# Performance work log

Hardware: AMD Instinct MI355X
Metric: run time of the kernel (lower is better)

Reference implementation:

```python
import jax, jax.numpy as jnp
import numpy as np

EPS_LN = 1e-05   # LayerNorm eps in SimpleCogVideoXLayerNormZero
EPS_QK = 1e-06   # RMSNorm eps for qk_norm

DIM = 2048
FFN = 8192
HEADS = 16
HEAD_DIM = DIM // HEADS
TEMB = 512
F, H, W = 4, 24, 24
SEQ = F * H * W  # 2304
B = 1


def _layernorm(x, weight, bias, eps):
    mu = jnp.mean(x, axis=-1, keepdims=True)
    var = jnp.mean((x - mu) ** 2, axis=-1, keepdims=True)
    return (x - mu) * jax.lax.rsqrt(var + eps) * weight + bias


def _rmsnorm(x, weight, eps):
    var = jnp.mean(x * x, axis=-1, keepdims=True)
    return x * jax.lax.rsqrt(var + eps) * weight


def _ln_zero(x, temb, lin_w, lin_b, n_w, n_b):
    # shift/scale/gate modulation from temb
    t = jax.nn.silu(temb) @ lin_w + lin_b          # [B, 3*dim]
    shift, scale, gate = jnp.split(t, 3, axis=1)
    xn = _layernorm(x, n_w, n_b, EPS_LN)
    return xn * (1.0 + scale)[:, None, :] + shift[:, None, :], gate[:, None, :]


def _rope(x, cos, sin):
    # x: [B, S, H, D]; cos/sin: [S, 1, D] broadcastable
    x1 = x[..., 0::2]
    x2 = x[..., 1::2]
    c = cos[..., 0::2]
    s = sin[..., 1::2]
    even = x1 * c - x2 * s
    odd = x1 * s + x2 * c
    return jnp.stack([even, odd], axis=-1).reshape(x.shape)


def _forward(hidden_states, ref_states, temb, cos_h, sin_h, cos_r, sin_r,
             ln1_lw, ln1_lb, ln1_nw, ln1_nb, ln2_lw, ln2_lb, ln2_nw, ln2_nb,
             wq, bq, wk, bk, wv, bv, nq_w, nk_w, wo, bo,
             ffn_w1, ffn_b1, ffn_w2, ffn_b2, f, h, w):
    b, s, dim = hidden_states.shape
    heads = HEADS
    hd = dim // heads
    scale = hd ** -0.5

    def qkv(x, cos, sin):
        q = _rmsnorm(x @ wq + bq, nq_w, EPS_QK)
        k = _rmsnorm(x @ wk + bk, nk_w, EPS_QK)
        v = x @ wv + bv
        q = q.reshape(b, s, heads, hd)
        k = k.reshape(b, s, heads, hd)
        v = v.reshape(b, s, heads, hd)
        q = _rope(q, cos, sin)
        k = _rope(k, cos, sin)
        return q, k, v

    def attn(nh, nr):
        q, k, v = qkv(nh, cos_h, sin_h)
        rq, rk, rv = qkv(nr, cos_r, sin_r)

        def combine(a, ra):
            a = a.reshape(b, f, h, w, heads, hd)
            ra = ra.reshape(b, f, h, w, heads, hd)
            c = jnp.concatenate([a, ra], axis=3)          # [b,f,h,2w,H,D]
            return c.reshape(b * f, h * 2 * w, heads, hd)  # [(bf),(h 2w),H,D]

        cq, ck, cv = combine(q, rq), combine(k, rk), combine(v, rv)
        logits = jnp.einsum('bqhd,bkhd->bhqk', cq, ck) * scale
        probs = jax.nn.softmax(logits, axis=-1)
        out = jnp.einsum('bhqk,bkhd->bqhd', probs, cv)
        out = out.reshape(b, f, h, 2 * w, heads, hd)
        ah = out[:, :, :, :w].reshape(b, s, dim)
        ar = out[:, :, :, w:].reshape(b, s, dim)
        return ah @ wo + bo, ar @ wo + bo

    def ffn(x):
        return jax.nn.gelu(x @ ffn_w1 + ffn_b1, approximate=True) @ ffn_w2 + ffn_b2

    norm_h, gate_h = _ln_zero(hidden_states, temb, ln1_lw, ln1_lb, ln1_nw, ln1_nb)
    norm_r, gate_r = _ln_zero(ref_states, temb, ln1_lw, ln1_lb, ln1_nw, ln1_nb)
    attn_h, attn_r = attn(norm_h, norm_r)

    hidden_states = hidden_states + gate_h * attn_h
    norm_h2, gate_ff = _ln_zero(hidden_states, temb, ln2_lw, ln2_lb, ln2_nw, ln2_nb)
    ref_states = ref_states + gate_r * attn_r
    norm_r2, gate_ff_r = _ln_zero(ref_states, temb, ln2_lw, ln2_lb, ln2_nw, ln2_nb)

    hidden_states = hidden_states + gate_ff * ffn(norm_h2)
    ref_states = ref_states + gate_ff_r * ffn(norm_r2)
    return hidden_states, ref_states


def setup_inputs() -> dict:
    key = jax.random.key(0)
    ks = jax.random.split(key, 24)
    std = 0.02
    inp = {
        'hidden_states': jax.random.normal(ks[0], (B, SEQ, DIM), jnp.float32),
        'ref_states': jax.random.normal(ks[1], (B, SEQ, DIM), jnp.float32),
        'temb': jax.random.normal(ks[2], (B, TEMB), jnp.float32),
        'cos_h': jax.random.uniform(ks[3], (SEQ, 1, HEAD_DIM), jnp.float32),
        'sin_h': jax.random.uniform(ks[4], (SEQ, 1, HEAD_DIM), jnp.float32),
        'cos_r': jax.random.uniform(ks[5], (SEQ, 1, HEAD_DIM), jnp.float32),
        'sin_r': jax.random.uniform(ks[6], (SEQ, 1, HEAD_DIM), jnp.float32),
        'ln1_lw': jax.random.normal(ks[7], (TEMB, 3 * DIM), jnp.float32) * std,
        'ln1_lb': jnp.zeros((3 * DIM,), jnp.float32),
        'ln1_nw': jnp.ones((DIM,), jnp.float32),
        'ln1_nb': jnp.zeros((DIM,), jnp.float32),
        'ln2_lw': jax.random.normal(ks[8], (TEMB, 3 * DIM), jnp.float32) * std,
        'ln2_lb': jnp.zeros((3 * DIM,), jnp.float32),
        'ln2_nw': jnp.ones((DIM,), jnp.float32),
        'ln2_nb': jnp.zeros((DIM,), jnp.float32),
        'wq': jax.random.normal(ks[9], (DIM, DIM), jnp.float32) * std,
        'bq': jnp.zeros((DIM,), jnp.float32),
        'wk': jax.random.normal(ks[10], (DIM, DIM), jnp.float32) * std,
        'bk': jnp.zeros((DIM,), jnp.float32),
        'wv': jax.random.normal(ks[11], (DIM, DIM), jnp.float32) * std,
        'bv': jnp.zeros((DIM,), jnp.float32),
        'nq_w': jnp.ones((DIM,), jnp.float32),
        'nk_w': jnp.ones((DIM,), jnp.float32),
        'wo': jax.random.normal(ks[12], (DIM, DIM), jnp.float32) * std,
        'bo': jnp.zeros((DIM,), jnp.float32),
        'ffn_w1': jax.random.normal(ks[13], (DIM, FFN), jnp.float32) * std,
        'ffn_b1': jnp.zeros((FFN,), jnp.float32),
        'ffn_w2': jax.random.normal(ks[14], (FFN, DIM), jnp.float32) * std,
        'ffn_b2': jnp.zeros((DIM,), jnp.float32),
        'f': F, 'h': H, 'w': W,
    }
    return inp


def reference(hidden_states, ref_states, temb, cos_h, sin_h, cos_r, sin_r,
              ln1_lw, ln1_lb, ln1_nw, ln1_nb, ln2_lw, ln2_lb, ln2_nw, ln2_nb,
              wq, bq, wk, bk, wv, bv, nq_w, nk_w, wo, bo,
              ffn_w1, ffn_b1, ffn_w2, ffn_b2, f, h, w):
    return _forward(hidden_states, ref_states, temb, cos_h, sin_h, cos_r, sin_r,
                    ln1_lw, ln1_lb, ln1_nw, ln1_nb, ln2_lw, ln2_lb, ln2_nw, ln2_nb,
                    wq, bq, wk, bk, wv, bv, nq_w, nk_w, wo, bo,
                    ffn_w1, ffn_b1, ffn_w2, ffn_b2, f, h, w)
```

## Files before the change

kernel.cpp:

```cpp
#include <hip/hip_runtime.h>

typedef unsigned int u32;
typedef unsigned short us16;
typedef __bf16 bf16x8 __attribute__((ext_vector_type(8)));
typedef float f32x4 __attribute__((ext_vector_type(4)));

constexpr int S    = 2304;
constexpr int S2   = 4608;
constexpr int D    = 2048;
constexpr int NQKV = 3 * D;
constexpr int NH   = 16;
constexpr int HD   = 128;
constexpr int FFN  = 8192;
constexpr int CT   = 1152;
constexpr float ATTN_SCALE = 0.08838834764831845f;

__device__ __forceinline__ us16 f2bf(float f) {
  u32 x = __float_as_uint(f);
  x += 0x7fffu + ((x >> 16) & 1u);
  return (us16)(x >> 16);
}
__device__ __forceinline__ float blk_sum256(float v, float* red, int tid) {
  #pragma unroll
  for (int o = 32; o; o >>= 1) v += __shfl_down(v, o, 64);
  __syncthreads();
  if ((tid & 63) == 0) red[tid >> 6] = v;
  __syncthreads();
  return red[0] + red[1] + red[2] + red[3];
}

typedef const __attribute__((address_space(1))) void* gas_ptr;
typedef __attribute__((address_space(3))) void* las_ptr;
__device__ __forceinline__ void gload16(const us16* g, us16* l) {
  __builtin_amdgcn_global_load_lds((gas_ptr)g, (las_ptr)l, 16, 0, 0);
}

__device__ __forceinline__ float gelu_tanh(float x) {
  float y = 0.7978845608028654f * (x + 0.044715f * x * x * x);
  float e = __expf(2.0f * y);
  float t = 1.0f - 2.0f / (e + 1.0f);
  return 0.5f * x * (1.0f + t);
}

__global__ __launch_bounds__(256) void transpose_cvt(
    const float* __restrict__ in, us16* __restrict__ out, int Kd, int Nd) {
  __shared__ float tile[32][33];
  int tx = threadIdx.x, ty = threadIdx.y;
  int n0 = blockIdx.x * 32, k0 = blockIdx.y * 32;
  #pragma unroll
  for (int i = 0; i < 4; i++)
    tile[ty + i * 8][tx] = in[(size_t)(k0 + ty + i * 8) * Nd + n0 + tx];
  __syncthreads();
  #pragma unroll
  for (int i = 0; i < 4; i++)
    out[(size_t)(n0 + ty + i * 8) * Kd + k0 + tx] = f2bf(tile[tx][ty + i * 8]);
}

__global__ __launch_bounds__(256) void temb_mod(
    const float* __restrict__ temb,
    const float* __restrict__ lw1, const float* __restrict__ lb1,
    const float* __restrict__ lw2, const float* __restrict__ lb2,
    float* __restrict__ t1, float* __restrict__ t2) {
  __shared__ float st[512];
  int tid = threadIdx.x;
  for (int i = tid; i < 512; i += 256) {
    float v = temb[i];
    st[i] = v / (1.0f + __expf(-v));
  }
  __syncthreads();
  int which = blockIdx.x / 24;
  int n = (blockIdx.x % 24) * 256 + tid;
  const float* lw = which ? lw2 : lw1;
  const float* lb = which ? lb2 : lb1;
  float acc = lb[n];
  #pragma unroll 4
  for (int k = 0; k < 512; k++) acc += st[k] * lw[(size_t)k * (3 * D) + n];
  (which ? t2 : t1)[n] = acc;
}

__global__ __launch_bounds__(256) void ln_mod(
    const float* __restrict__ x, const float* __restrict__ t,
    const float* __restrict__ nw, const float* __restrict__ nb,
    us16* __restrict__ out) {
  __shared__ float red[4];
  int tok = blockIdx.x, tid = threadIdx.x;
  const float* xr = x + (size_t)tok * D;
  float v[8];
  float4 a = *(const float4*)(xr + tid * 8);
  float4 b = *(const float4*)(xr + tid * 8 + 4);
  v[0]=a.x; v[1]=a.y; v[2]=a.z; v[3]=a.w; v[4]=b.x; v[5]=b.y; v[6]=b.z; v[7]=b.w;
  float s = 0;
  #pragma unroll
  for (int i = 0; i < 8; i++) s += v[i];
  float mu = blk_sum256(s, red, tid) * (1.0f / D);
  float sq = 0;
  #pragma unroll
  for (int i = 0; i < 8; i++) { float d = v[i] - mu; sq += d * d; }
  float var = blk_sum256(sq, red, tid) * (1.0f / D);
  float rinv = rsqrtf(var + 1e-5f);
  int n = tid * 8;
  us16 o[8];
  #pragma unroll
  for (int i = 0; i < 8; i++) {
    float xn = (v[i] - mu) * rinv * nw[n + i] + nb[n + i];
    float y = xn * (1.0f + t[D + n + i]) + t[n + i];
    o[i] = f2bf(y);
  }
  *(uint4*)(out + (size_t)tok * D + n) = *(uint4*)o;
}

template <int EPI>
__global__ __launch_bounds__(256) void gemm128(
    const us16* __restrict__ A, const us16* __restrict__ BT,
    const float* __restrict__ b0, const float* __restrict__ b1,
    const float* __restrict__ b2, int bmask, void* __restrict__ Cout,
    int M, int N, int K) {
  __shared__ __align__(16) us16 As[128 * 32];
  __shared__ __align__(16) us16 Bs[128 * 32];
  const int tid = threadIdx.x;

  const int nbx = N >> 7;
  const int nwg = nbx * (M >> 7);
  int bid = (int)blockIdx.x;
  bid = (bid & 7) * (nwg >> 3) + (bid >> 3);
  const int by = bid / nbx;
  const int m0 = by << 7;
  const int n0 = (bid - by * nbx) << 7;

  const int srow = tid >> 2;
  const int scol = (tid & 3) << 3;
  const us16* Ap = A + (size_t)(m0 + srow) * K + scol;
  const us16* Bp = BT + (size_t)(n0 + srow) * K + scol;
  const size_t rstep = (size_t)64 * K;
  us16* lA = As + ((tid >> 6) << 9);
  us16* lB = Bs + ((tid >> 6) << 9);

  const int w = tid >> 6, l = tid & 63;
  const int wr = (w >> 1) << 6, wc = (w & 1) << 6;
  const int m = l & 15, quad = l >> 4;
  const us16* Ard = As + (wr + m) * 32 + quad * 8;
  const us16* Brd = Bs + (wc + m) * 32 + quad * 8;

  f32x4 acc[4][4] = {};
  for (int k0 = 0; k0 < K; k0 += 32) {
    __syncthreads();
    gload16(Ap + k0, lA);
    gload16(Ap + rstep + k0, lA + 2048);
    gload16(Bp + k0, lB);
    gload16(Bp + rstep + k0, lB + 2048);
    __syncthreads();
    bf16x8 af[4], bf[4];
    #pragma unroll
    for (int i = 0; i < 4; i++) {
      af[i] = *(const bf16x8*)(Ard + i * 512);
      bf[i] = *(const bf16x8*)(Brd + i * 512);
    }
    #pragma unroll
    for (int mi = 0; mi < 4; mi++)
      #pragma unroll
      for (int ni = 0; ni < 4; ni++)
        acc[mi][ni] = __builtin_amdgcn_mfma_f32_16x16x32_bf16(
            af[mi], bf[ni], acc[mi][ni], 0, 0, 0);
  }

  const float* bp = b0;
  if (b1) { int seg = (n0 + wc) >> 11; if (seg == 1) bp = b1; else if (seg >= 2) bp = b2; }

  const int r0 = m0 + wr + (quad << 2);
  #pragma unroll
  for (int ni = 0; ni < 4; ni++) {
    const int col = n0 + wc + ni * 16 + m;
    const float bv = bp ? bp[col & bmask] : 0.0f;
    #pragma unroll
    for (int mi = 0; mi < 4; mi++) {
      const int row = r0 + mi * 16;
      #pragma unroll
      for (int r = 0; r < 4; r++) {
        float y = acc[mi][ni][r] + bv;
        if constexpr (EPI == 1) {
          ((us16*)Cout)[(size_t)(row + r) * N + col] = f2bf(gelu_tanh(y));
        } else {
          ((float*)Cout)[(size_t)(row + r) * N + col] = y;
        }
      }
    }
  }
}

__global__ __launch_bounds__(256) void qkv_scatter(
    const float* __restrict__ raw, const float* __restrict__ nw,
    const float* __restrict__ cos_h, const float* __restrict__ sin_h,
    const float* __restrict__ cos_r, const float* __restrict__ sin_r,
    us16* __restrict__ out, int mode) {
  __shared__ float red[4];
  int t = blockIdx.x, tid = threadIdx.x;
  int is_ref = t >= S;
  int tt = is_ref ? t - S : t;
  const float* xr = raw + (size_t)t * NQKV + mode * D;
  float v[8];
  float4 a = *(const float4*)(xr + tid * 8);
  float4 b = *(const float4*)(xr + tid * 8 + 4);
  v[0]=a.x; v[1]=a.y; v[2]=a.z; v[3]=a.w; v[4]=b.x; v[5]=b.y; v[6]=b.z; v[7]=b.w;
  int n = tid * 8;
  int head = n >> 7, d = n & 127;
  float o8[8];
  if (mode < 2) {
    float s = 0;
    #pragma unroll
    for (int i = 0; i < 8; i++) s += v[i] * v[i];
    float tot = blk_sum256(s, red, tid);
    float rinv = rsqrtf(tot * (1.0f / D) + 1e-6f);
    const float* cr = (is_ref ? cos_r : cos_h) + (size_t)tt * HD;
    const float* sr = (is_ref ? sin_r : sin_h) + (size_t)tt * HD;
    #pragma unroll
    for (int p = 0; p < 4; p++) {
      float x1 = v[2 * p] * rinv * nw[n + 2 * p];
      float x2 = v[2 * p + 1] * rinv * nw[n + 2 * p + 1];
      float ce = cr[d + 2 * p];
      float so = sr[d + 2 * p + 1];
      o8[2 * p]     = x1 * ce - x2 * so;
      o8[2 * p + 1] = x1 * so + x2 * ce;
    }
    if (mode == 0) {
      #pragma unroll
      for (int i = 0; i < 8; i++) o8[i] *= ATTN_SCALE;
    }
  } else {
    #pragma unroll
    for (int i = 0; i < 8; i++) o8[i] = v[i];
  }
  int f = tt / 576, rem = tt % 576;
  int row = rem / 24, col = rem - row * 24;
  int comb = row * 48 + col + (is_ref ? 24 : 0);
  size_t oidx = ((size_t)(f * NH + head) * CT + comb) * HD + d;
  us16 packed[8];
  #pragma unroll
  for (int i = 0; i < 8; i++) packed[i] = f2bf(o8[i]);
  *(uint4*)(out + oidx) = *(uint4*)packed;
}

__global__ __launch_bounds__(256) void attn_mfma(
    const us16* __restrict__ qc, const us16* __restrict__ kc,
    const us16* __restrict__ vc, us16* __restrict__ ah, us16* __restrict__ ar) {
  __shared__ __align__(16) us16 Qs[64][136];
  __shared__ __align__(16) us16 Ks[64][136];
  __shared__ __align__(16) us16 Vts[128][72];
  __shared__ __align__(16) us16 Ps[4][16][72];
  int tid = threadIdx.x;
  int w = tid >> 6, l = tid & 63;
  int m = l & 15, quad = l >> 4;
  int bx = blockIdx.x;
  int fh = bx / 18, qt = bx % 18;
  size_t base = (size_t)fh * CT * HD;
  int qbase = qt * 64;

  {
    int row = tid >> 2, c0 = (tid & 3) * 32;
    const us16* src = qc + base + (size_t)(qbase + row) * HD + c0;
    #pragma unroll
    for (int j = 0; j < 4; j++)
      *(uint4*)&Qs[row][c0 + 8 * j] = *(const uint4*)(src + 8 * j);
  }
  __syncthreads();
  bf16x8 qf[4];
  #pragma unroll
  for (int c = 0; c < 4; c++)
    qf[c] = *(const bf16x8*)&Qs[16 * w + m][32 * c + quad * 8];

  float mo[4] = {-1e30f, -1e30f, -1e30f, -1e30f};
  float li[4] = {0.f, 0.f, 0.f, 0.f};
  f32x4 o[8] = {};

  #pragma unroll 1
  for (int kb = 0; kb < CT; kb += 64) {
    __syncthreads();
    {
      int row = tid >> 2, c0 = (tid & 3) * 32;
      const us16* src = kc + base + (size_t)(kb + row) * HD + c0;
      #pragma unroll
      for (int j = 0; j < 4; j++)
        *(uint4*)&Ks[row][c0 + 8 * j] = *(const uint4*)(src + 8 * j);
    }
    {
      int key = tid & 63, d0 = (tid >> 6) * 32;
      const us16* src = vc + base + (size_t)(kb + key) * HD + d0;
      #pragma unroll
      for (int j = 0; j < 4; j++) {
        uint4 vv = *(const uint4*)(src + 8 * j);
        us16 tmp[8];
        *(uint4*)tmp = vv;
        #pragma unroll
        for (int i = 0; i < 8; i++) Vts[d0 + 8 * j + i][key] = tmp[i];
      }
    }
    __syncthreads();
    f32x4 s[4] = {};
    #pragma unroll
    for (int kt = 0; kt < 4; kt++) {
      #pragma unroll
      for (int c = 0; c < 4; c++) {
        bf16x8 kf = *(const bf16x8*)&Ks[kt * 16 + m][32 * c + quad * 8];
        s[kt] = __builtin_amdgcn_mfma_f32_16x16x32_bf16(qf[c], kf, s[kt], 0, 0, 0);
      }
    }
    float al[4];
    #pragma unroll
    for (int r = 0; r < 4; r++) {
      float v = fmaxf(fmaxf(s[0][r], s[1][r]), fmaxf(s[2][r], s[3][r]));
      #pragma unroll
      for (int off = 8; off; off >>= 1) v = fmaxf(v, __shfl_xor(v, off));
      float mn = fmaxf(mo[r], v);
      al[r] = __expf(mo[r] - mn);
      mo[r] = mn;
      float ps = 0.f;
      #pragma unroll
      for (int kt = 0; kt < 4; kt++) {
        float p = __expf(s[kt][r] - mn);
        s[kt][r] = p;
        ps += p;
      }
      #pragma unroll
      for (int off = 8; off; off >>= 1) ps += __shfl_xor(ps, off);
      li[r] = li[r] * al[r] + ps;
    }
    #pragma unroll
    for (int kt = 0; kt < 4; kt++)
      #pragma unroll
      for (int r = 0; r < 4; r++)
        Ps[w][quad * 4 + r][kt * 16 + m] = f2bf(s[kt][r]);
    #pragma unroll
    for (int dt = 0; dt < 8; dt++)
      #pragma unroll
      for (int r = 0; r < 4; r++)
        o[dt][r] *= al[r];
    __syncthreads();
    #pragma unroll
    for (int c = 0; c < 2; c++) {
      bf16x8 pf = *(const bf16x8*)&Ps[w][m][32 * c + quad * 8];
      #pragma unroll
      for (int dt = 0; dt < 8; dt++) {
        bf16x8 vf = *(const bf16x8*)&Vts[dt * 16 + m][32 * c + quad * 8];
        o[dt] = __builtin_amdgcn_mfma_f32_16x16x32_bf16(pf, vf, o[dt], 0, 0, 0);
      }
    }
  }
  int f = fh >> 4, h = fh & 15;
  #pragma unroll
  for (int r = 0; r < 4; r++) {
    float rl = 1.0f / li[r];
    int q = qbase + 16 * w + quad * 4 + r;
    int row = q / 48, cc = q - row * 48;
    int isr = cc >= 24;
    int tok = f * 576 + row * 24 + (isr ? cc - 24 : cc);
    us16* dstp = (isr ? ar : ah) + (size_t)tok * D + h * HD;
    #pragma unroll
    for (int dt = 0; dt < 8; dt++)
      dstp[dt * 16 + m] = f2bf(o[dt][r] * rl);
  }
}

__global__ __launch_bounds__(256) void residual_gate(
    const float* __restrict__ x, const float* __restrict__ attn,
    const float* __restrict__ gate, float* __restrict__ out) {
  size_t i = ((size_t)blockIdx.x * 256 + threadIdx.x) * 4;
  float4 xv = *(const float4*)(x + i);
  float4 av = *(const float4*)(attn + i);
  int n = (int)(i & (D - 1));
  float4 g = *(const float4*)(gate + n);
  float4 o;
  o.x = xv.x + g.x * av.x;
  o.y = xv.y + g.y * av.y;
  o.z = xv.z + g.z * av.z;
  o.w = xv.w + g.w * av.w;
  *(float4*)(out + i) = o;
}

constexpr size_t O_WQ   = 0;
constexpr size_t O_WK   = 8388608;
constexpr size_t O_WV   = 16777216;
constexpr size_t O_WO   = 25165824;
constexpr size_t O_NHR  = 33603584;
constexpr size_t O_RAW  = 52477952;
constexpr size_t O_QC   = 165724160;
constexpr size_t O_KC   = 184598528;
constexpr size_t O_VC   = 203472896;
constexpr size_t O_T1   = 222347264;
constexpr size_t O_T2   = 222371840;
constexpr size_t O_AH   = O_RAW;
constexpr size_t O_ATTN = O_RAW + 18874368;
constexpr size_t O_W1T  = 0;
constexpr size_t O_W2T  = 33554432;
constexpr size_t O_N2   = 67108864;
constexpr size_t O_MIDB = 85983232;
constexpr size_t O_FOUT = 161480704;

extern "C" void kernel_launch(void* const* d_in, const int* in_sizes, int n_in,
                              void* d_out, int out_size, void* d_ws, size_t ws_size,
                              hipStream_t stream) {
  (void)in_sizes; (void)n_in; (void)out_size; (void)ws_size;
  const float* hidden = (const float*)d_in[0];
  const float* refs   = (const float*)d_in[1];
  const float* temb   = (const float*)d_in[2];
  const float* cos_h  = (const float*)d_in[3];
  const float* sin_h  = (const float*)d_in[4];
  const float* cos_r  = (const float*)d_in[5];
  const float* sin_r  = (const float*)d_in[6];
  const float* ln1_lw = (const float*)d_in[7];
  const float* ln1_lb = (const float*)d_in[8];
  const float* ln1_nw = (const float*)d_in[9];
  const float* ln1_nb = (const float*)d_in[10];
  const float* ln2_lw = (const float*)d_in[11];
  const float* ln2_lb = (const float*)d_in[12];
  const float* ln2_nw = (const float*)d_in[13];
  const float* ln2_nb = (const float*)d_in[14];
  const float* wq = (const float*)d_in[15];
  const float* bq = (const float*)d_in[16];
  const float* wk = (const float*)d_in[17];
  const float* bk = (const float*)d_in[18];
  const float* wv = (const float*)d_in[19];
  const float* bv = (const float*)d_in[20];
  const float* nq_w = (const float*)d_in[21];
  const float* nk_w = (const float*)d_in[22];
  const float* wo = (const float*)d_in[23];
  const float* bo = (const float*)d_in[24];
  const float* ffn_w1 = (const float*)d_in[25];
  const float* ffn_b1 = (const float*)d_in[26];
  const float* ffn_w2 = (const float*)d_in[27];
  const float* ffn_b2 = (const float*)d_in[28];

  char* ws = (char*)d_ws;
  us16* p_wq  = (us16*)(ws + O_WQ);
  us16* p_wk  = (us16*)(ws + O_WK);
  us16* p_wv  = (us16*)(ws + O_WV);
  us16* p_wo  = (us16*)(ws + O_WO);
  us16* p_nhr = (us16*)(ws + O_NHR);
  float* p_raw = (float*)(ws + O_RAW);
  us16* p_qc  = (us16*)(ws + O_QC);
  us16* p_kc  = (us16*)(ws + O_KC);
  us16* p_vc  = (us16*)(ws + O_VC);
  float* p_t1 = (float*)(ws + O_T1);
  float* p_t2 = (float*)(ws + O_T2);
  us16* p_ah  = (us16*)(ws + O_AH);
  us16* p_ar  = p_ah + (size_t)S * D;
  float* p_attn = (float*)(ws + O_ATTN);
  us16* p_w1t = (us16*)(ws + O_W1T);
  us16* p_w2t = (us16*)(ws + O_W2T);
  us16* p_n2  = (us16*)(ws + O_N2);
  us16* p_midb = (us16*)(ws + O_MIDB);
  float* p_fout = (float*)(ws + O_FOUT);
  float* outh = (float*)d_out;
  float* outr = (float*)d_out + (size_t)S * D;

  constexpr int G_QKV  = (NQKV / 128) * (S2 / 128);
  constexpr int G_WO   = (D / 128) * (S2 / 128);
  constexpr int G_FFN1 = (FFN / 128) * (S2 / 128);
  constexpr int G_FFN2 = G_WO;

  dim3 tb(32, 8);
  transpose_cvt<<<dim3(64, 64), tb, 0, stream>>>(wq, p_wq, D, D);
  transpose_cvt<<<dim3(64, 64), tb, 0, stream>>>(wk, p_wk, D, D);
  transpose_cvt<<<dim3(64, 64), tb, 0, stream>>>(wv, p_wv, D, D);
  transpose_cvt<<<dim3(64, 64), tb, 0, stream>>>(wo, p_wo, D, D);
  temb_mod<<<48, 256, 0, stream>>>(temb, ln1_lw, ln1_lb, ln2_lw, ln2_lb, p_t1, p_t2);
  ln_mod<<<S, 256, 0, stream>>>(hidden, p_t1, ln1_nw, ln1_nb, p_nhr);
  ln_mod<<<S, 256, 0, stream>>>(refs,   p_t1, ln1_nw, ln1_nb, p_nhr + (size_t)S * D);
  gemm128<0><<<G_QKV, 256, 0, stream>>>(p_nhr, p_wq, bq, bk, bv, D - 1,
                                        p_raw, S2, NQKV, D);
  qkv_scatter<<<S2, 256, 0, stream>>>(p_raw, nq_w, cos_h, sin_h, cos_r, sin_r, p_qc, 0);
  qkv_scatter<<<S2, 256, 0, stream>>>(p_raw, nk_w, cos_h, sin_h, cos_r, sin_r, p_kc, 1);
  qkv_scatter<<<S2, 256, 0, stream>>>(p_raw, nq_w, cos_h, sin_h, cos_r, sin_r, p_vc, 2);
  attn_mfma<<<64 * 18, 256, 0, stream>>>(p_qc, p_kc, p_vc, p_ah, p_ar);
  gemm128<0><<<G_WO, 256, 0, stream>>>(p_ah, p_wo, bo, nullptr, nullptr, D - 1,
                                       p_attn, S2, D, D);
  residual_gate<<<4608, 256, 0, stream>>>(hidden, p_attn, p_t1 + 2 * D, outh);
  residual_gate<<<4608, 256, 0, stream>>>(refs, p_attn + (size_t)S * D,
                                          p_t1 + 2 * D, outr);
  transpose_cvt<<<dim3(256, 64), tb, 0, stream>>>(ffn_w1, p_w1t, D, FFN);
  transpose_cvt<<<dim3(64, 256), tb, 0, stream>>>(ffn_w2, p_w2t, FFN, D);
  ln_mod<<<S2, 256, 0, stream>>>((const float*)d_out, p_t2, ln2_nw, ln2_nb, p_n2);
  gemm128<1><<<G_FFN1, 256, 0, stream>>>(p_n2, p_w1t, ffn_b1, nullptr, nullptr,
                                         FFN - 1, p_midb, S2, FFN, D);
  gemm128<0><<<G_FFN2, 256, 0, stream>>>(p_midb, p_w2t, ffn_b2, nullptr, nullptr,
                                         D - 1, p_fout, S2, D, FFN);
  residual_gate<<<9216, 256, 0, stream>>>((const float*)d_out, p_fout,
                                          p_t2 + 2 * D, (float*)d_out);
}
```

Measured before the change: 1.352 ms.

## Triple-buffer GEMM LDS loads and fuse residual gate into GEMM epilogue

The GEMM main loop now uses three LDS stages with async global-to-LDS loads issued two tiles ahead. Each iteration has one barrier with a partial vmcnt wait instead of two full syncthreads, so load latency overlaps with MFMA work. The gated residual add is folded into the Wo and FFN2 GEMM epilogues, which drops the fp32 intermediate buffers and separate elementwise passes. The three qkv_scatter launches are merged into one. This triples LDS use per block, which may lower occupancy. The epilogue also does uncoalesced scalar reads of the residual.

```diff
diff --git a/kernel.cpp b/kernel.cpp
--- a/kernel.cpp
+++ b/kernel.cpp
@@ -114,9 +114,11 @@
     const us16* __restrict__ A, const us16* __restrict__ BT,
     const float* __restrict__ b0, const float* __restrict__ b1,
     const float* __restrict__ b2, int bmask, void* __restrict__ Cout,
-    int M, int N, int K) {
-  __shared__ __align__(16) us16 As[128 * 32];
-  __shared__ __align__(16) us16 Bs[128 * 32];
+    int M, int N, int K,
+    const float* __restrict__ xa, const float* __restrict__ xb,
+    const float* __restrict__ gate) {
+  __shared__ __align__(16) us16 As[3][128 * 32];
+  __shared__ __align__(16) us16 Bs[3][128 * 32];
   const int tid = threadIdx.x;
 
   const int nbx = N >> 7;
@@ -132,28 +134,44 @@
   const us16* Ap = A + (size_t)(m0 + srow) * K + scol;
   const us16* Bp = BT + (size_t)(n0 + srow) * K + scol;
   const size_t rstep = (size_t)64 * K;
-  us16* lA = As + ((tid >> 6) << 9);
-  us16* lB = Bs + ((tid >> 6) << 9);
+  const int wvofs = (tid >> 6) << 9;
 
   const int w = tid >> 6, l = tid & 63;
   const int wr = (w >> 1) << 6, wc = (w & 1) << 6;
   const int m = l & 15, quad = l >> 4;
-  const us16* Ard = As + (wr + m) * 32 + quad * 8;
-  const us16* Brd = Bs + (wc + m) * 32 + quad * 8;
+  const int aoff = (wr + m) * 32 + quad * 8;
+  const int boff = (wc + m) * 32 + quad * 8;
+
+  us16 *p0a = &As[0][0], *p1a = &As[1][0], *p2a = &As[2][0];
+  us16 *p0b = &Bs[0][0], *p1b = &Bs[1][0], *p2b = &Bs[2][0];
+
+  gload16(Ap,          p0a + wvofs);
+  gload16(Ap + rstep,  p0a + wvofs + 2048);
+  gload16(Bp,          p0b + wvofs);
+  gload16(Bp + rstep,  p0b + wvofs + 2048);
+  gload16(Ap + 32,         p1a + wvofs);
+  gload16(Ap + rstep + 32, p1a + wvofs + 2048);
+  gload16(Bp + 32,         p1b + wvofs);
+  gload16(Bp + rstep + 32, p1b + wvofs + 2048);
+  asm volatile("s_waitcnt vmcnt(4)" ::: "memory");
+  __builtin_amdgcn_s_barrier();
+  __builtin_amdgcn_sched_barrier(0);
 
   f32x4 acc[4][4] = {};
   for (int k0 = 0; k0 < K; k0 += 32) {
-    __syncthreads();
-    gload16(Ap + k0, lA);
-    gload16(Ap + rstep + k0, lA + 2048);
-    gload16(Bp + k0, lB);
-    gload16(Bp + rstep + k0, lB + 2048);
-    __syncthreads();
+    const int k2 = k0 + 64;
+    if (k2 < K) {
+      gload16(Ap + k2,         p2a + wvofs);
+      gload16(Ap + rstep + k2, p2a + wvofs + 2048);
+      gload16(Bp + k2,         p2b + wvofs);
+      gload16(Bp + rstep + k2, p2b + wvofs + 2048);
+    }
+    __builtin_amdgcn_sched_barrier(0);
     bf16x8 af[4], bf[4];
     #pragma unroll
     for (int i = 0; i < 4; i++) {
-      af[i] = *(const bf16x8*)(Ard + i * 512);
-      bf[i] = *(const bf16x8*)(Brd + i * 512);
+      af[i] = *(const bf16x8*)(p0a + aoff + i * 512);
+      bf[i] = *(const bf16x8*)(p0b + boff + i * 512);
     }
     #pragma unroll
     for (int mi = 0; mi < 4; mi++)
@@ -161,6 +179,14 @@
       for (int ni = 0; ni < 4; ni++)
         acc[mi][ni] = __builtin_amdgcn_mfma_f32_16x16x32_bf16(
             af[mi], bf[ni], acc[mi][ni], 0, 0, 0);
+    __builtin_amdgcn_sched_barrier(0);
+    if (k2 < K) asm volatile("s_waitcnt vmcnt(4)" ::: "memory");
+    else        asm volatile("s_waitcnt vmcnt(0)" ::: "memory");
+    __builtin_amdgcn_s_barrier();
+    __builtin_amdgcn_sched_barrier(0);
+    us16* t;
+    t = p0a; p0a = p1a; p1a = p2a; p2a = t;
+    t = p0b; p0b = p1b; p1b = p2b; p2b = t;
   }
 
   const float* bp = b0;
@@ -179,6 +205,11 @@
         float y = acc[mi][ni][r] + bv;
         if constexpr (EPI == 1) {
           ((us16*)Cout)[(size_t)(row + r) * N + col] = f2bf(gelu_tanh(y));
+        } else if constexpr (EPI == 2) {
+          const int rr = row + r;
+          const float xv = (rr < S) ? xa[(size_t)rr * N + col]
+                                    : xb[(size_t)(rr - S) * N + col];
+          ((float*)Cout)[(size_t)rr * N + col] = xv + gate[col & bmask] * y;
         } else {
           ((float*)Cout)[(size_t)(row + r) * N + col] = y;
         }
@@ -188,12 +219,17 @@
 }
 
 __global__ __launch_bounds__(256) void qkv_scatter(
-    const float* __restrict__ raw, const float* __restrict__ nw,
+    const float* __restrict__ raw,
+    const float* __restrict__ nq_w, const float* __restrict__ nk_w,
     const float* __restrict__ cos_h, const float* __restrict__ sin_h,
     const float* __restrict__ cos_r, const float* __restrict__ sin_r,
-    us16* __restrict__ out, int mode) {
+    us16* __restrict__ qc, us16* __restrict__ kc, us16* __restrict__ vc) {
   __shared__ float red[4];
-  int t = blockIdx.x, tid = threadIdx.x;
+  int bid = blockIdx.x, tid = threadIdx.x;
+  int mode = bid / S2;
+  int t = bid - mode * S2;
+  us16* out = mode == 0 ? qc : (mode == 1 ? kc : vc);
+  const float* nw = mode == 1 ? nk_w : nq_w;
   int is_ref = t >= S;
   int tt = is_ref ? t - S : t;
   const float* xr = raw + (size_t)t * NQKV + mode * D;
@@ -359,22 +395,6 @@
   }
 }
 
-__global__ __launch_bounds__(256) void residual_gate(
-    const float* __restrict__ x, const float* __restrict__ attn,
-    const float* __restrict__ gate, float* __restrict__ out) {
-  size_t i = ((size_t)blockIdx.x * 256 + threadIdx.x) * 4;
-  float4 xv = *(const float4*)(x + i);
-  float4 av = *(const float4*)(attn + i);
-  int n = (int)(i & (D - 1));
-  float4 g = *(const float4*)(gate + n);
-  float4 o;
-  o.x = xv.x + g.x * av.x;
-  o.y = xv.y + g.y * av.y;
-  o.z = xv.z + g.z * av.z;
-  o.w = xv.w + g.w * av.w;
-  *(float4*)(out + i) = o;
-}
-
 constexpr size_t O_WQ   = 0;
 constexpr size_t O_WK   = 8388608;
 constexpr size_t O_WV   = 16777216;
@@ -387,12 +407,10 @@
 constexpr size_t O_T1   = 222347264;
 constexpr size_t O_T2   = 222371840;
 constexpr size_t O_AH   = O_RAW;
-constexpr size_t O_ATTN = O_RAW + 18874368;
 constexpr size_t O_W1T  = 0;
 constexpr size_t O_W2T  = 33554432;
 constexpr size_t O_N2   = 67108864;
 constexpr size_t O_MIDB = 85983232;
-constexpr size_t O_FOUT = 161480704;
 
 extern "C" void kernel_launch(void* const* d_in, const int* in_sizes, int n_in,
                               void* d_out, int out_size, void* d_ws, size_t ws_size,
@@ -442,14 +460,11 @@
   float* p_t2 = (float*)(ws + O_T2);
   us16* p_ah  = (us16*)(ws + O_AH);
   us16* p_ar  = p_ah + (size_t)S * D;
-  float* p_attn = (float*)(ws + O_ATTN);
   us16* p_w1t = (us16*)(ws + O_W1T);
   us16* p_w2t = (us16*)(ws + O_W2T);
   us16* p_n2  = (us16*)(ws + O_N2);
   us16* p_midb = (us16*)(ws + O_MIDB);
-  float* p_fout = (float*)(ws + O_FOUT);
-  float* outh = (float*)d_out;
-  float* outr = (float*)d_out + (size_t)S * D;
+  float* outd = (float*)d_out;
 
   constexpr int G_QKV  = (NQKV / 128) * (S2 / 128);
   constexpr int G_WO   = (D / 128) * (S2 / 128);
@@ -465,23 +480,22 @@
   ln_mod<<<S, 256, 0, stream>>>(hidden, p_t1, ln1_nw, ln1_nb, p_nhr);
   ln_mod<<<S, 256, 0, stream>>>(refs,   p_t1, ln1_nw, ln1_nb, p_nhr + (size_t)S * D);
   gemm128<0><<<G_QKV, 256, 0, stream>>>(p_nhr, p_wq, bq, bk, bv, D - 1,
-                                        p_raw, S2, NQKV, D);
-  qkv_scatter<<<S2, 256, 0, stream>>>(p_raw, nq_w, cos_h, sin_h, cos_r, sin_r, p_qc, 0);
-  qkv_scatter<<<S2, 256, 0, stream>>>(p_raw, nk_w, cos_h, sin_h, cos_r, sin_r, p_kc, 1);
-  qkv_scatter<<<S2, 256, 0, stream>>>(p_raw, nq_w, cos_h, sin_h, cos_r, sin_r, p_vc, 2);
+                                        p_raw, S2, NQKV, D,
+                                        nullptr, nullptr, nullptr);
+  qkv_scatter<<<3 * S2, 256, 0, stream>>>(p_raw, nq_w, nk_w,
+                                          cos_h, sin_h, cos_r, sin_r,
+                                          p_qc, p_kc, p_vc);
   attn_mfma<<<64 * 18, 256, 0, stream>>>(p_qc, p_kc, p_vc, p_ah, p_ar);
-  gemm128<0><<<G_WO, 256, 0, stream>>>(p_ah, p_wo, bo, nullptr, nullptr, D - 1,
-                                       p_attn, S2, D, D);
-  residual_gate<<<4608, 256, 0, stream>>>(hidden, p_attn, p_t1 + 2 * D, outh);
-  residual_gate<<<4608, 256, 0, stream>>>(refs, p_attn + (size_t)S * D,
-                                          p_t1 + 2 * D, outr);
+  gemm128<2><<<G_WO, 256, 0, stream>>>(p_ah, p_wo, bo, nullptr, nullptr, D - 1,
+                                       outd, S2, D, D,
+                                       hidden, refs, p_t1 + 2 * D);
   transpose_cvt<<<dim3(256, 64), tb, 0, stream>>>(ffn_w1, p_w1t, D, FFN);
   transpose_cvt<<<dim3(64, 256), tb, 0, stream>>>(ffn_w2, p_w2t, FFN, D);
-  ln_mod<<<S2, 256, 0, stream>>>((const float*)d_out, p_t2, ln2_nw, ln2_nb, p_n2);
+  ln_mod<<<S2, 256, 0, stream>>>(outd, p_t2, ln2_nw, ln2_nb, p_n2);
   gemm128<1><<<G_FFN1, 256, 0, stream>>>(p_n2, p_w1t, ffn_b1, nullptr, nullptr,
-                                         FFN - 1, p_midb, S2, FFN, D);
-  gemm128<0><<<G_FFN2, 256, 0, stream>>>(p_midb, p_w2t, ffn_b2, nullptr, nullptr,
-                                         D - 1, p_fout, S2, D, FFN);
-  residual_gate<<<9216, 256, 0, stream>>>((const float*)d_out, p_fout,
-                                          p_t2 + 2 * D, (float*)d_out);
-}
+                                         FFN - 1, p_midb, S2, FFN, D,
+                                         nullptr, nullptr, nullptr);
+  gemm128<2><<<G_FFN2, 256, 0, stream>>>(p_midb, p_w2t, ffn_b2, nullptr, nullptr,
+                                         D - 1, outd, S2, D, FFN,
+                                         outd, outd + (size_t)S * D, p_t2 + 2 * D);
+}
```

New measurement: 1.471 ms. 8.8% more time.
